# Kernel optimization log

Measured on AMD Instinct MI355X. Metric: run time of the kernel, lower is better.

The kernel has to match this reference:

```python
import jax, jax.numpy as jnp
import numpy as np

DIM_IN, DIM_OUT, DIM_CTX = 128, 256, 259
B, N, S_CTX = 32, 2048, 1
BN_EPS = 1e-5


def setup_inputs() -> dict:
    key = jax.random.key(0)
    ks = jax.random.split(key, 12)
    s = 0.02
    return {
        "ctx": jax.random.normal(ks[0], (B, S_CTX, DIM_CTX), jnp.float32),
        "x": jax.random.normal(ks[1], (B, N, DIM_IN), jnp.float32),
        "W_layer": jax.random.normal(ks[2], (DIM_OUT, DIM_IN), jnp.float32) * s,
        "b_layer": jax.random.normal(ks[3], (DIM_OUT,), jnp.float32) * s,
        "W_hbias": jax.random.normal(ks[4], (DIM_OUT, DIM_CTX), jnp.float32) * s,
        "W_gate": jax.random.normal(ks[5], (DIM_OUT, DIM_CTX), jnp.float32) * s,
        "b_gate": jax.random.normal(ks[6], (DIM_OUT,), jnp.float32) * s,
        "W_k": jax.random.normal(ks[7], (DIM_OUT, DIM_CTX - 3), jnp.float32) * s,
        "W_v": jax.random.normal(ks[8], (DIM_OUT, DIM_CTX - 3), jnp.float32) * s,
        "W_tc": jax.random.normal(ks[9], (DIM_OUT, DIM_OUT), jnp.float32) * s,
        "b_tc": jax.random.normal(ks[10], (DIM_OUT,), jnp.float32) * s,
        "bn_gamma": jnp.ones((N,), jnp.float32),
        "bn_beta": jnp.zeros((N,), jnp.float32),
    }


def reference(ctx, x, W_layer, b_layer, W_hbias, W_gate, b_gate, W_k, W_v, W_tc, b_tc, bn_gamma, bn_beta):
    # FiLM gate / bias from context: [B, 1, dim_out]
    gate = jax.nn.sigmoid(jnp.einsum('bsc,oc->bso', ctx, W_gate) + b_gate)
    bias = jnp.einsum('bsc,oc->bso', ctx, W_hbias)

    # main linear: [B, N, dim_out]
    x1 = jnp.einsum('bni,oi->bno', x, W_layer) + b_layer

    # channel attention from shape context (drop last 3 ctx dims)
    shape = ctx[:, :, : ctx.shape[2] - 3]                      # [B, S, C-3]
    shape_k = jnp.einsum('bsc,oc->bos', shape, W_k)            # [B, dim_out, S]
    shape_v = jnp.einsum('bsc,oc->bso', shape, W_v)            # [B, S, dim_out]
    energy = jnp.einsum('bos,bse->boe', shape_k, shape_v)      # [B, dim_out, dim_out]
    attention = jax.nn.softmax(energy, axis=-1)
    attention = attention / (1e-9 + attention.sum(axis=1, keepdims=True))

    # channel mixing: [B, N, dim_out]
    x_r = jnp.einsum('bno,boe->bne', x1, attention)

    # trans_conv + BatchNorm1d(N) (train-mode batch stats over dims (0, 2)) + ReLU
    t = jnp.einsum('bno,eo->bne', x1 - x_r, W_tc) + b_tc       # [B, N, dim_out]
    mean = t.mean(axis=(0, 2), keepdims=True)                  # per point-channel
    var = t.var(axis=(0, 2), keepdims=True)                    # biased variance
    t = (t - mean) * jax.lax.rsqrt(var + BN_EPS)
    t = t * bn_gamma[None, :, None] + bn_beta[None, :, None]
    x_r = jax.nn.relu(t)

    xo = x1 + x_r
    return xo * gate + bias
```

## Files before the change

kernel.cpp:

```cpp
#include <hip/hip_runtime.h>
#include <hip/hip_bf16.h>

#define BB   32
#define NN   2048
#define DIN  128
#define DOUT 256
#define DCTX 259

#define OFF_AB   0u
#define OFF_WMB  16777216u
#define OFF_WLB  17301504u
#define OFF_WLTB 17317888u
#define OFF_WTCB 17334272u
#define OFF_G    17367040u
#define OFF_HB   17375232u
#define OFF_TB   17383424u
#define OFF_P1   17655296u
#define OFF_P2   17720832u
#define OFF_KS   17786368u
#define OFF_VS   17794560u
#define OFF_CNT  17802752u

typedef short bf16x8 __attribute__((ext_vector_type(8)));
typedef float f32x4  __attribute__((ext_vector_type(4)));

static __device__ inline unsigned short f2bf(float f) {
    __hip_bfloat16 h = __float2bfloat16(f);
    return *(unsigned short*)&h;
}
static __device__ inline float bf2f(unsigned short u) {
    unsigned v = ((unsigned)u) << 16;
    float f;
    __builtin_memcpy(&f, &v, 4);
    return f;
}

__global__ __launch_bounds__(256) void kW(const float* __restrict__ Wl,
                                          const float* __restrict__ Wtc,
                                          const float* __restrict__ Wk,
                                          const float* __restrict__ Wv,
                                          const float* __restrict__ Wg,
                                          const float* __restrict__ Whb,
                                          const float* __restrict__ ctx,
                                          const float* __restrict__ bg,
                                          float* __restrict__ ws) {
    const unsigned bb = blockIdx.x, t = threadIdx.x;
    __shared__ float ctxs[32][260];
    __shared__ float wt[16][260];

    if (bb < 8u) {
        unsigned base = bb * 8192u;
        unsigned short* dst = (unsigned short*)(ws + OFF_WTCB);
#pragma unroll
        for (int j = 0; j < 32; j++) {
            unsigned i = base + (unsigned)j * 256u + t;
            dst[i] = f2bf(Wtc[i]);
        }
        return;
    } else if (bb == 8u) {
        unsigned short* dst = (unsigned short*)(ws + OFF_WLTB);
        for (unsigned idx = t; idx < 32768u; idx += 256u) {
            unsigned i = idx >> 8, o = idx & 255u;
            dst[idx] = f2bf(Wl[o * 128u + i]);
        }
        return;
    } else if (bb == 9u) {
        unsigned short* dst = (unsigned short*)(ws + OFF_WLB);
        for (unsigned idx = t; idx < 32768u; idx += 256u) dst[idx] = f2bf(Wl[idx]);
        return;
    } else if (bb == 74u) {
        unsigned* c = (unsigned*)(ws + OFF_CNT);
        for (unsigned i = t; i < 1024u; i += 256u) c[i] = 0u;
        return;
    }

    const int j = bb - 10;
    const int m = j >> 4;
    const int o0 = (j & 15) * 16;
    const float* Wm; int C;
    if (m == 0)      { Wm = Wk;  C = 256; }
    else if (m == 1) { Wm = Wv;  C = 256; }
    else if (m == 2) { Wm = Wg;  C = DCTX; }
    else             { Wm = Whb; C = DCTX; }

    for (int i = t; i < 32 * 260; i += 256) {
        int b2 = i / 260, c = i - b2 * 260;
        ctxs[b2][c] = (c < DCTX) ? ctx[b2 * DCTX + c] : 0.f;
    }
    for (int i = t; i < 16 * C; i += 256) {
        int r = i / C, c = i - r * C;
        wt[r][c] = Wm[(size_t)(o0 + r) * C + c];
    }
    __syncthreads();

    const int ol = t & 15, b2 = t >> 4;
    float s0 = 0.f, s1 = 0.f;
#pragma unroll 8
    for (int c = 0; c < C; c++) {
        float w = wt[ol][c];
        s0 += w * ctxs[b2][c];
        s1 += w * ctxs[b2 + 16][c];
    }
    const int o = o0 + ol;
    if (m == 0) {
        ws[OFF_KS + b2 * DOUT + o] = s0;
        ws[OFF_KS + (b2 + 16) * DOUT + o] = s1;
    } else if (m == 1) {
        ws[OFF_VS + b2 * DOUT + o] = s0;
        ws[OFF_VS + (b2 + 16) * DOUT + o] = s1;
    } else if (m == 2) {
        float bgo = bg[o];
        ws[OFF_G + b2 * DOUT + o] = 1.f / (1.f + __expf(-(s0 + bgo)));
        ws[OFF_G + (b2 + 16) * DOUT + o] = 1.f / (1.f + __expf(-(s1 + bgo)));
    } else {
        ws[OFF_HB + b2 * DOUT + o] = s0;
        ws[OFF_HB + (b2 + 16) * DOUT + o] = s1;
    }
}

__global__ __launch_bounds__(1024) void kP(float* __restrict__ ws) {
    const int b = blockIdx.x, t = threadIdx.x;
    const int o = t & 255, q = t >> 8;
    __shared__ __align__(16) float ks[256], vs[256], rms[256], ris[256];
    __shared__ float pm[1024], ps[1024];
    if (t < 256)            ks[t] = ws[OFF_KS + b * DOUT + t];
    else if (t < 512)       vs[t - 256] = ws[OFF_VS + b * DOUT + (t - 256)];
    __syncthreads();

    const float ko = ks[o];
    const float4* vs4 = (const float4*)vs;
    float pmax = -1e30f;
#pragma unroll 4
    for (int j = q * 16; j < q * 16 + 16; j++) {
        float4 v = vs4[j];
        pmax = fmaxf(pmax, fmaxf(fmaxf(ko * v.x, ko * v.y), fmaxf(ko * v.z, ko * v.w)));
    }
    pm[q * 256 + o] = pmax;
    __syncthreads();
    float m = fmaxf(fmaxf(pm[o], pm[256 + o]), fmaxf(pm[512 + o], pm[768 + o]));
    float psum = 0.f;
#pragma unroll 4
    for (int j = q * 16; j < q * 16 + 16; j++) {
        float4 v = vs4[j];
        psum += __expf(ko * v.x - m) + __expf(ko * v.y - m)
              + __expf(ko * v.z - m) + __expf(ko * v.w - m);
    }
    ps[q * 256 + o] = psum;
    __syncthreads();
    float ri = 1.f / (ps[o] + ps[256 + o] + ps[512 + o] + ps[768 + o]);
    if (q == 0) { rms[o] = m; ris[o] = ri; }
    __syncthreads();

    const float ve = vs[o];
    float cp = 0.f;
#pragma unroll 4
    for (int o2 = q * 64; o2 < q * 64 + 64; o2++)
        cp += __expf(ks[o2] * ve - rms[o2]) * ris[o2];
    pm[q * 256 + o] = cp;
    __syncthreads();
    float ci = 1.f / (1e-9f + pm[o] + pm[256 + o] + pm[512 + o] + pm[768 + o]);
    unsigned short* Ab = (unsigned short*)(ws + OFF_AB) + (size_t)b * 65536u;
#pragma unroll 4
    for (int o2 = q * 64; o2 < q * 64 + 64; o2++) {
        float a = __expf(ks[o2] * ve - rms[o2]) * ris[o2] * ci;
        Ab[o2 * 256 + o] = f2bf(a);
    }
}

__global__ __launch_bounds__(512) void k45(const float* __restrict__ bl,
                                           const float* __restrict__ btc,
                                           float* __restrict__ ws) {
    const int t = threadIdx.x, wid = t >> 6, l = t & 63;
    const int b = blockIdx.y, et = blockIdx.x;
    const int lrow = l & 15, lk = l >> 4;
    __shared__ unsigned short Mt[64 * 256];
    const unsigned short* Wtcb = (const unsigned short*)(ws + OFF_WTCB);

    {
        const unsigned short* Ab = (const unsigned short*)(ws + OFF_AB) + (size_t)b * 65536u;
        const int w_r = wid >> 2, w_c = wid & 3;
        const int rbase = et * 64 + w_r * 32;
        const int colbase = w_c * 64;
        f32x4 acc[2][4];
#pragma unroll
        for (int i = 0; i < 2; i++)
#pragma unroll
            for (int c = 0; c < 4; c++) acc[i][c] = (f32x4){0.f, 0.f, 0.f, 0.f};
        const unsigned short* ar0 = Wtcb + (rbase + lrow) * 256;
#pragma unroll
        for (int kk = 0; kk < 8; kk++) {
            int ko = kk * 32 + lk * 8;
            bf16x8 a0 = *(const bf16x8*)(ar0 + ko);
            bf16x8 a1 = *(const bf16x8*)(ar0 + 16 * 256 + ko);
            bf16x8 bfr[4];
#pragma unroll
            for (int c = 0; c < 4; c++)
                bfr[c] = *(const bf16x8*)(Ab + (colbase + c * 16 + lrow) * 256 + ko);
#pragma unroll
            for (int c = 0; c < 4; c++) {
                acc[0][c] = __builtin_amdgcn_mfma_f32_16x16x32_bf16(a0, bfr[c], acc[0][c], 0, 0, 0);
                acc[1][c] = __builtin_amdgcn_mfma_f32_16x16x32_bf16(a1, bfr[c], acc[1][c], 0, 0, 0);
            }
        }
#pragma unroll
        for (int t2 = 0; t2 < 2; t2++)
#pragma unroll
            for (int c = 0; c < 4; c++)
#pragma unroll
                for (int r = 0; r < 4; r++) {
                    int grow = rbase + t2 * 16 + lk * 4 + r;
                    int col = colbase + c * 16 + lrow;
                    float idv = bf2f(Wtcb[grow * 256 + col]);
                    int rl = grow - et * 64;
                    Mt[rl * 256 + (col ^ ((rl & 7) << 3))] = f2bf(idv - acc[t2][c][r]);
                }
    }
    __syncthreads();
    {
        const unsigned short* Wltb = (const unsigned short*)(ws + OFF_WLTB);
        const int w_r = wid >> 2, w_c = wid & 3;
        const int rl0 = w_r * 32;
        const int colb = w_c * 32;
        f32x4 acc[2][2];
#pragma unroll
        for (int i = 0; i < 2; i++)
#pragma unroll
            for (int c = 0; c < 2; c++) acc[i][c] = (f32x4){0.f, 0.f, 0.f, 0.f};
        const int arow0 = rl0 + lrow, arow1 = rl0 + 16 + lrow;
        const int asw0 = (arow0 & 7) << 3, asw1 = (arow1 & 7) << 3;
#pragma unroll
        for (int kk = 0; kk < 8; kk++) {
            int ko = kk * 32 + lk * 8;
            bf16x8 a0 = *(const bf16x8*)(Mt + arow0 * 256 + (ko ^ asw0));
            bf16x8 a1 = *(const bf16x8*)(Mt + arow1 * 256 + (ko ^ asw1));
            bf16x8 bfr[2];
#pragma unroll
            for (int c = 0; c < 2; c++)
                bfr[c] = *(const bf16x8*)(Wltb + (colb + c * 16 + lrow) * 256 + ko);
#pragma unroll
            for (int c = 0; c < 2; c++) {
                acc[0][c] = __builtin_amdgcn_mfma_f32_16x16x32_bf16(a0, bfr[c], acc[0][c], 0, 0, 0);
                acc[1][c] = __builtin_amdgcn_mfma_f32_16x16x32_bf16(a1, bfr[c], acc[1][c], 0, 0, 0);
            }
        }
        unsigned short* WMBp = (unsigned short*)(ws + OFF_WMB) + (size_t)b * 32768u;
#pragma unroll
        for (int t2 = 0; t2 < 2; t2++)
#pragma unroll
            for (int c = 0; c < 2; c++)
#pragma unroll
                for (int r = 0; r < 4; r++) {
                    int row = et * 64 + rl0 + t2 * 16 + lk * 4 + r;
                    int col = colb + c * 16 + lrow;
                    WMBp[row * 128 + col] = f2bf(acc[t2][c][r]);
                }
    }
    if (t < 64) {
        const int rl = t;
        const int sw = (rl & 7) << 3;
        float s = 0.f;
#pragma unroll 4
        for (int j = 0; j < 32; j++) {
            bf16x8 ch = *(const bf16x8*)(Mt + rl * 256 + ((j * 8) ^ sw));
#pragma unroll
            for (int u = 0; u < 8; u++) s += bl[j * 8 + u] * bf2f((unsigned short)ch[u]);
        }
        ws[OFF_TB + b * DOUT + et * 64 + rl] = s + btc[et * 64 + rl];
    }
}

#define LDP 136

__global__ __launch_bounds__(256) void kFS(const float* __restrict__ x,
                                           const float* __restrict__ bl,
                                           const float* __restrict__ gamma,
                                           const float* __restrict__ beta,
                                           float* __restrict__ out,
                                           float* __restrict__ ws) {
    const int t = threadIdx.x;
    const int wid = t >> 6, l = t & 63;
    const int b = blockIdx.x;
    const int nt = blockIdx.y;
    const int n0 = nt * 64;
    const int lrow = l & 15, lk = l >> 4;
    __shared__ unsigned short xs[64 * LDP];
    __shared__ float sp1[4][64], sp2[4][64];
    __shared__ float scs[64], shs[64];

    const float4* xg = (const float4*)(x + (size_t)(b * NN + n0) * DIN);
#pragma unroll
    for (int it = 0; it < 8; it++) {
        int idx = it * 256 + t;
        int row = idx >> 5, kq = idx & 31;
        float4 v = xg[idx];
        ushort4 u;
        u.x = f2bf(v.x); u.y = f2bf(v.y); u.z = f2bf(v.z); u.w = f2bf(v.w);
        *(ushort4*)(xs + row * LDP + kq * 4) = u;
    }
    __syncthreads();

    const int colbase = wid * 64;

    f32x4 acc[4][4];
#pragma unroll
    for (int rt = 0; rt < 4; rt++)
#pragma unroll
        for (int ct = 0; ct < 4; ct++) acc[rt][ct] = (f32x4){0.f, 0.f, 0.f, 0.f};
    {
        const unsigned short* wbM = (const unsigned short*)(ws + OFF_WMB) + (size_t)b * 32768u;
#pragma unroll
        for (int kk = 0; kk < 4; kk++) {
            int ko = kk * 32 + lk * 8;
            bf16x8 a[4];
#pragma unroll
            for (int rt = 0; rt < 4; rt++)
                a[rt] = *(const bf16x8*)(xs + (rt * 16 + lrow) * LDP + ko);
            bf16x8 bf[4];
#pragma unroll
            for (int ct = 0; ct < 4; ct++)
                bf[ct] = *(const bf16x8*)(wbM + (size_t)(colbase + ct * 16 + lrow) * DIN + ko);
#pragma unroll
            for (int rt = 0; rt < 4; rt++)
#pragma unroll
                for (int ct = 0; ct < 4; ct++)
                    acc[rt][ct] = __builtin_amdgcn_mfma_f32_16x16x32_bf16(a[rt], bf[ct], acc[rt][ct], 0, 0, 0);
        }
#pragma unroll
        for (int ct = 0; ct < 4; ct++) {
            float bv = ws[OFF_TB + b * DOUT + colbase + ct * 16 + lrow];
#pragma unroll
            for (int rt = 0; rt < 4; rt++)
#pragma unroll
                for (int r = 0; r < 4; r++) acc[rt][ct][r] += bv;
        }
    }

    {
        float s1[4][4], s2[4][4];
#pragma unroll
        for (int rt = 0; rt < 4; rt++)
#pragma unroll
            for (int r = 0; r < 4; r++) { s1[rt][r] = 0.f; s2[rt][r] = 0.f; }
#pragma unroll
        for (int rt = 0; rt < 4; rt++)
#pragma unroll
            for (int ct = 0; ct < 4; ct++)
#pragma unroll
                for (int r = 0; r < 4; r++) {
                    float v = acc[rt][ct][r];
                    s1[rt][r] += v; s2[rt][r] += v * v;
                }
#pragma unroll
        for (int off = 1; off < 16; off <<= 1) {
#pragma unroll
            for (int rt = 0; rt < 4; rt++)
#pragma unroll
                for (int r = 0; r < 4; r++) {
                    s1[rt][r] += __shfl_xor(s1[rt][r], off, 64);
                    s2[rt][r] += __shfl_xor(s2[rt][r], off, 64);
                }
        }
        if (lrow == 0) {
#pragma unroll
            for (int rt = 0; rt < 4; rt++)
#pragma unroll
                for (int r = 0; r < 4; r++) {
                    int nidx = rt * 16 + lk * 4 + r;
                    sp1[wid][nidx] = s1[rt][r];
                    sp2[wid][nidx] = s2[rt][r];
                }
        }
    }
    __syncthreads();
    if (t < 64) {
        float S1 = sp1[0][t] + sp1[1][t] + sp1[2][t] + sp1[3][t];
        float S2 = sp2[0][t] + sp2[1][t] + sp2[2][t] + sp2[3][t];
        ws[OFF_P1 + (size_t)b * NN + n0 + t] = S1;
        ws[OFF_P2 + (size_t)b * NN + n0 + t] = S2;
    }
    __syncthreads();

    unsigned* cnt = (unsigned*)(ws + OFF_CNT) + (size_t)nt * 32;
    if (t == 0)
        __hip_atomic_fetch_add(cnt, 1u, __ATOMIC_RELEASE, __HIP_MEMORY_SCOPE_AGENT);

    f32x4 acc0[4][4];
#pragma unroll
    for (int rt = 0; rt < 4; rt++)
#pragma unroll
        for (int ct = 0; ct < 4; ct++) acc0[rt][ct] = (f32x4){0.f, 0.f, 0.f, 0.f};
    {
        const unsigned short* wbL = (const unsigned short*)(ws + OFF_WLB);
#pragma unroll
        for (int kk = 0; kk < 4; kk++) {
            int ko = kk * 32 + lk * 8;
            bf16x8 a[4];
#pragma unroll
            for (int rt = 0; rt < 4; rt++)
                a[rt] = *(const bf16x8*)(xs + (rt * 16 + lrow) * LDP + ko);
            bf16x8 bf[4];
#pragma unroll
            for (int ct = 0; ct < 4; ct++)
                bf[ct] = *(const bf16x8*)(wbL + (size_t)(colbase + ct * 16 + lrow) * DIN + ko);
#pragma unroll
            for (int rt = 0; rt < 4; rt++)
#pragma unroll
                for (int ct = 0; ct < 4; ct++)
                    acc0[rt][ct] = __builtin_amdgcn_mfma_f32_16x16x32_bf16(a[rt], bf[ct], acc0[rt][ct], 0, 0, 0);
        }
#pragma unroll
        for (int ct = 0; ct < 4; ct++) {
            float bv = bl[colbase + ct * 16 + lrow];
#pragma unroll
            for (int rt = 0; rt < 4; rt++)
#pragma unroll
                for (int r = 0; r < 4; r++) acc0[rt][ct][r] += bv;
        }
    }

    if (t == 0) {
        while (__hip_atomic_load(cnt, __ATOMIC_ACQUIRE, __HIP_MEMORY_SCOPE_AGENT) < (unsigned)BB)
            __builtin_amdgcn_s_sleep(32);
    }
    __syncthreads();

    {
        int n = t & 63, g = t >> 6;
        float S1 = 0.f, S2 = 0.f;
#pragma unroll
        for (int b2 = g * 8; b2 < g * 8 + 8; b2++) {
            S1 += ws[OFF_P1 + (size_t)b2 * NN + n0 + n];
            S2 += ws[OFF_P2 + (size_t)b2 * NN + n0 + n];
        }
        sp1[g][n] = S1; sp2[g][n] = S2;
    }
    __syncthreads();
    if (t < 64) {
        float S1 = sp1[0][t] + sp1[1][t] + sp1[2][t] + sp1[3][t];
        float S2 = sp2[0][t] + sp2[1][t] + sp2[2][t] + sp2[3][t];
        float mean = S1 * (1.f / 8192.f);
        float var  = S2 * (1.f / 8192.f) - mean * mean;
        float sc = gamma[n0 + t] * rsqrtf(fmaxf(var, 0.f) + 1e-5f);
        scs[t] = sc;
        shs[t] = beta[n0 + t] - mean * sc;
    }
    __syncthreads();

    float gv[4], hbv[4];
#pragma unroll
    for (int ct = 0; ct < 4; ct++) {
        int o = colbase + ct * 16 + lrow;
        gv[ct]  = ws[OFF_G  + b * DOUT + o];
        hbv[ct] = ws[OFF_HB + b * DOUT + o];
    }
#pragma unroll
    for (int rt = 0; rt < 4; rt++)
#pragma unroll
        for (int r = 0; r < 4; r++) {
            int nidx = rt * 16 + lk * 4 + r;
            float sc = scs[nidx], sh = shs[nidx];
            int n = n0 + nidx;
#pragma unroll
            for (int ct = 0; ct < 4; ct++) {
                int o = colbase + ct * 16 + lrow;
                float rv = fmaxf(acc[rt][ct][r] * sc + sh, 0.f);
                out[(size_t)((b * NN + n) * DOUT) + o] = (acc0[rt][ct][r] + rv) * gv[ct] + hbv[ct];
            }
        }
}

extern "C" void kernel_launch(void* const* d_in, const int* in_sizes, int n_in,
                              void* d_out, int out_size, void* d_ws, size_t ws_size,
                              hipStream_t stream) {
    const float* ctx   = (const float*)d_in[0];
    const float* x     = (const float*)d_in[1];
    const float* Wl    = (const float*)d_in[2];
    const float* bl    = (const float*)d_in[3];
    const float* Whb   = (const float*)d_in[4];
    const float* Wg    = (const float*)d_in[5];
    const float* bg    = (const float*)d_in[6];
    const float* Wk    = (const float*)d_in[7];
    const float* Wv    = (const float*)d_in[8];
    const float* Wtc   = (const float*)d_in[9];
    const float* btc   = (const float*)d_in[10];
    const float* gamma = (const float*)d_in[11];
    const float* beta  = (const float*)d_in[12];
    float* out = (float*)d_out;
    float* ws  = (float*)d_ws;

    kW  <<<75, 256, 0, stream>>>(Wl, Wtc, Wk, Wv, Wg, Whb, ctx, bg, ws);
    kP  <<<BB, 1024, 0, stream>>>(ws);
    k45 <<<dim3(4, BB), 512, 0, stream>>>(bl, btc, ws);
    kFS <<<dim3(BB, 32), 256, 0, stream>>>(x, bl, gamma, beta, out, ws);
}
```

Before: 208.0 us.

## Fuse attention-softmax kernel into channel-mix GEMM, generating attention tiles in LDS

Removes the separate per-batch softmax kernel that wrote a bf16 256x256 attention matrix per batch to global workspace. Each block of the fused kernel now recomputes the row max and sum and the column normalisation itself, then builds each 32-wide K slice of the attention matrix directly in shared memory before the MFMA. This saves one launch and the global write and read of the attention matrices. In exchange, the softmax statistics are computed redundantly by 4 blocks per batch, and two extra barriers per K step are added.

```diff
diff --git a/kernel.cpp b/kernel.cpp
--- a/kernel.cpp
+++ b/kernel.cpp
@@ -7,7 +7,6 @@
 #define DOUT 256
 #define DCTX 259
 
-#define OFF_AB   0u
 #define OFF_WMB  16777216u
 #define OFF_WLB  17301504u
 #define OFF_WLTB 17317888u
@@ -118,67 +117,58 @@
     }
 }
 
-__global__ __launch_bounds__(1024) void kP(float* __restrict__ ws) {
-    const int b = blockIdx.x, t = threadIdx.x;
-    const int o = t & 255, q = t >> 8;
-    __shared__ __align__(16) float ks[256], vs[256], rms[256], ris[256];
-    __shared__ float pm[1024], ps[1024];
-    if (t < 256)            ks[t] = ws[OFF_KS + b * DOUT + t];
-    else if (t < 512)       vs[t - 256] = ws[OFF_VS + b * DOUT + (t - 256)];
-    __syncthreads();
-
-    const float ko = ks[o];
-    const float4* vs4 = (const float4*)vs;
-    float pmax = -1e30f;
-#pragma unroll 4
-    for (int j = q * 16; j < q * 16 + 16; j++) {
-        float4 v = vs4[j];
-        pmax = fmaxf(pmax, fmaxf(fmaxf(ko * v.x, ko * v.y), fmaxf(ko * v.z, ko * v.w)));
-    }
-    pm[q * 256 + o] = pmax;
-    __syncthreads();
-    float m = fmaxf(fmaxf(pm[o], pm[256 + o]), fmaxf(pm[512 + o], pm[768 + o]));
-    float psum = 0.f;
-#pragma unroll 4
-    for (int j = q * 16; j < q * 16 + 16; j++) {
-        float4 v = vs4[j];
-        psum += __expf(ko * v.x - m) + __expf(ko * v.y - m)
-              + __expf(ko * v.z - m) + __expf(ko * v.w - m);
-    }
-    ps[q * 256 + o] = psum;
-    __syncthreads();
-    float ri = 1.f / (ps[o] + ps[256 + o] + ps[512 + o] + ps[768 + o]);
-    if (q == 0) { rms[o] = m; ris[o] = ri; }
-    __syncthreads();
-
-    const float ve = vs[o];
-    float cp = 0.f;
-#pragma unroll 4
-    for (int o2 = q * 64; o2 < q * 64 + 64; o2++)
-        cp += __expf(ks[o2] * ve - rms[o2]) * ris[o2];
-    pm[q * 256 + o] = cp;
-    __syncthreads();
-    float ci = 1.f / (1e-9f + pm[o] + pm[256 + o] + pm[512 + o] + pm[768 + o]);
-    unsigned short* Ab = (unsigned short*)(ws + OFF_AB) + (size_t)b * 65536u;
-#pragma unroll 4
-    for (int o2 = q * 64; o2 < q * 64 + 64; o2++) {
-        float a = __expf(ks[o2] * ve - rms[o2]) * ris[o2] * ci;
-        Ab[o2 * 256 + o] = f2bf(a);
-    }
-}
-
-__global__ __launch_bounds__(512) void k45(const float* __restrict__ bl,
-                                           const float* __restrict__ btc,
-                                           float* __restrict__ ws) {
+__global__ __launch_bounds__(512) void kQ(const float* __restrict__ bl,
+                                          const float* __restrict__ btc,
+                                          float* __restrict__ ws) {
     const int t = threadIdx.x, wid = t >> 6, l = t & 63;
     const int b = blockIdx.y, et = blockIdx.x;
     const int lrow = l & 15, lk = l >> 4;
     __shared__ unsigned short Mt[64 * 256];
+    __shared__ unsigned short Abc[256 * 40];
+    __shared__ __align__(16) float ks[256], vs[256], rms[256], ris[256], ci[256];
+    __shared__ float pm[512], ps[512];
     const unsigned short* Wtcb = (const unsigned short*)(ws + OFF_WTCB);
 
-    {
-        const unsigned short* Ab = (const unsigned short*)(ws + OFF_AB) + (size_t)b * 65536u;
-        const int w_r = wid >> 2, w_c = wid & 3;
+    if (t < 256)      ks[t] = ws[OFF_KS + b * DOUT + t];
+    else              vs[t - 256] = ws[OFF_VS + b * DOUT + (t - 256)];
+    __syncthreads();
+    const int o = t & 255, q = t >> 8;
+    {
+        const float ko_ = ks[o];
+        const float4* vs4 = (const float4*)vs;
+        float pmax = -1e30f;
+#pragma unroll 4
+        for (int j = q * 32; j < q * 32 + 32; j++) {
+            float4 v = vs4[j];
+            pmax = fmaxf(pmax, fmaxf(fmaxf(ko_ * v.x, ko_ * v.y), fmaxf(ko_ * v.z, ko_ * v.w)));
+        }
+        pm[t] = pmax;
+        __syncthreads();
+        float m = fmaxf(pm[o], pm[256 + o]);
+        float psum = 0.f;
+#pragma unroll 4
+        for (int j = q * 32; j < q * 32 + 32; j++) {
+            float4 v = vs4[j];
+            psum += __expf(ko_ * v.x - m) + __expf(ko_ * v.y - m)
+                  + __expf(ko_ * v.z - m) + __expf(ko_ * v.w - m);
+        }
+        ps[t] = psum;
+        __syncthreads();
+        if (q == 0) { rms[o] = m; ris[o] = 1.f / (ps[o] + ps[256 + o]); }
+        __syncthreads();
+        const float ve = vs[o];
+        float cp = 0.f;
+#pragma unroll 4
+        for (int o2 = q * 128; o2 < q * 128 + 128; o2++)
+            cp += __expf(ks[o2] * ve - rms[o2]) * ris[o2];
+        pm[t] = cp;
+        __syncthreads();
+        if (q == 0) ci[o] = 1.f / (1e-9f + pm[o] + pm[256 + o]);
+        __syncthreads();
+    }
+
+    const int w_r = wid >> 2, w_c = wid & 3;
+    {
         const int rbase = et * 64 + w_r * 32;
         const int colbase = w_c * 64;
         f32x4 acc[2][4];
@@ -187,20 +177,28 @@
 #pragma unroll
             for (int c = 0; c < 4; c++) acc[i][c] = (f32x4){0.f, 0.f, 0.f, 0.f};
         const unsigned short* ar0 = Wtcb + (rbase + lrow) * 256;
-#pragma unroll
+        const int o2 = t & 255, h = t >> 8;
+        const float k2 = ks[o2], rm = rms[o2], ri = ris[o2];
         for (int kk = 0; kk < 8; kk++) {
+#pragma unroll 8
+            for (int j = 0; j < 16; j++) {
+                int e = kk * 32 + h * 16 + j;
+                Abc[o2 * 40 + h * 16 + j] = f2bf(__expf(k2 * vs[e] - rm) * ri * ci[e]);
+            }
+            __syncthreads();
             int ko = kk * 32 + lk * 8;
             bf16x8 a0 = *(const bf16x8*)(ar0 + ko);
             bf16x8 a1 = *(const bf16x8*)(ar0 + 16 * 256 + ko);
             bf16x8 bfr[4];
 #pragma unroll
             for (int c = 0; c < 4; c++)
-                bfr[c] = *(const bf16x8*)(Ab + (colbase + c * 16 + lrow) * 256 + ko);
+                bfr[c] = *(const bf16x8*)(Abc + (colbase + c * 16 + lrow) * 40 + lk * 8);
 #pragma unroll
             for (int c = 0; c < 4; c++) {
                 acc[0][c] = __builtin_amdgcn_mfma_f32_16x16x32_bf16(a0, bfr[c], acc[0][c], 0, 0, 0);
                 acc[1][c] = __builtin_amdgcn_mfma_f32_16x16x32_bf16(a1, bfr[c], acc[1][c], 0, 0, 0);
             }
+            __syncthreads();
         }
 #pragma unroll
         for (int t2 = 0; t2 < 2; t2++)
@@ -218,7 +216,6 @@
     __syncthreads();
     {
         const unsigned short* Wltb = (const unsigned short*)(ws + OFF_WLTB);
-        const int w_r = wid >> 2, w_c = wid & 3;
         const int rl0 = w_r * 32;
         const int colb = w_c * 32;
         f32x4 acc[2][2];
@@ -489,7 +486,6 @@
     float* ws  = (float*)d_ws;
 
     kW  <<<75, 256, 0, stream>>>(Wl, Wtc, Wk, Wv, Wg, Whb, ctx, bg, ws);
-    kP  <<<BB, 1024, 0, stream>>>(ws);
-    k45 <<<dim3(4, BB), 512, 0, stream>>>(bl, btc, ws);
+    kQ  <<<dim3(4, BB), 512, 0, stream>>>(bl, btc, ws);
     kFS <<<dim3(BB, 32), 256, 0, stream>>>(x, bl, gamma, beta, out, ws);
 }
```

New measurement: 200.3 us. -3.7%, faster.
